# Kernel optimization log

Hardware: AMD Instinct MI355X
Metric: run time of the kernel (lower is better)

## Reference

```python
import jax, jax.numpy as jnp
import numpy as np

B, S, D, H = 2, 2048, 1024, 16
DK = D // H

def setup_inputs() -> dict:
    key = jax.random.key(0)
    ks = jax.random.split(key, 9)
    sc = 1.0 / np.sqrt(D)
    return {
        "query": jax.random.normal(ks[0], (B, S, D), jnp.float32),
        "key_": jax.random.normal(ks[1], (B, S, D), jnp.float32),
        "value": jax.random.normal(ks[2], (B, S, D), jnp.float32),
        "Wq": jax.random.normal(ks[3], (D, D), jnp.float32) * sc,
        "bq": jnp.zeros((D,), jnp.float32),
        "Wk": jax.random.normal(ks[4], (D, D), jnp.float32) * sc,
        "bk": jnp.zeros((D,), jnp.float32),
        "Wv": jax.random.normal(ks[5], (D, D), jnp.float32) * sc,
        "bv": jnp.zeros((D,), jnp.float32),
    }

def reference(query, key_, value, Wq, bq, Wk, bk, Wv, bv):
    # QKV projections -> [B, H, S, DK]
    def heads(x, W, b):
        return (x @ W + b).reshape(B, S, H, DK).transpose(0, 2, 1, 3)
    q = heads(query, Wq, bq)
    k = heads(key_, Wk, bk)
    v = heads(value, Wv, bv)
    scores = jnp.einsum('bhsd,bhtd->bhst', q, k) / jnp.sqrt(jnp.float32(DK))
    attn = jax.nn.softmax(scores, axis=-1)  # dropout = identity (eval)
    ctx = jnp.einsum('bhst,bhtd->bhsd', attn, v)
    return ctx.transpose(0, 2, 1, 3).reshape(B, S, D)
```

## Files before the change

### kernel.cpp

```cpp
#include <hip/hip_runtime.h>
#include <hip/hip_bf16.h>

typedef __bf16 bf16x4 __attribute__((ext_vector_type(4)));
typedef __bf16 bf16x8 __attribute__((ext_vector_type(8)));
typedef float  f32x4  __attribute__((ext_vector_type(4)));
typedef float  f32x16 __attribute__((ext_vector_type(16)));

constexpr int B = 2, S = 2048, D = 1024, H = 16, DK = 64;
constexpr int M = B * S;
constexpr int BH = B * H;

__device__ inline float fexp2(float x) {
#if __has_builtin(__builtin_amdgcn_exp2f)
  return __builtin_amdgcn_exp2f(x);
#else
  return exp2f(x);
#endif
}
__device__ inline float frcp(float x) {
#if __has_builtin(__builtin_amdgcn_rcpf)
  return __builtin_amdgcn_rcpf(x);
#else
  return 1.0f / x;
#endif
}
__device__ inline unsigned pk2(float lo, float hi) {
  union { __bf16 h[2]; unsigned u; } x;
  x.h[0] = (__bf16)lo; x.h[1] = (__bf16)hi;
  return x.u;
}

__global__ __launch_bounds__(256) void wtrans3(const float* __restrict__ w0,
                                               const float* __restrict__ w1,
                                               const float* __restrict__ w2,
                                               __bf16* __restrict__ t0,
                                               __bf16* __restrict__ t1,
                                               __bf16* __restrict__ t2) {
  int z = blockIdx.z;
  const float* W = z == 0 ? w0 : z == 1 ? w1 : w2;
  __bf16* WT = z == 0 ? t0 : z == 1 ? t1 : t2;
  __shared__ float t[32][33];
  int tx = threadIdx.x & 31, ty0 = threadIdx.x >> 5;
  int n0 = blockIdx.x * 32, k0 = blockIdx.y * 32;
#pragma unroll
  for (int i = 0; i < 4; ++i)
    t[ty0 + i * 8][tx] = W[(size_t)(k0 + ty0 + i * 8) * D + n0 + tx];
  __syncthreads();
#pragma unroll
  for (int i = 0; i < 4; ++i)
    WT[(size_t)(n0 + ty0 + i * 8) * D + k0 + tx] = (__bf16)t[tx][ty0 + i * 8];
}

constexpr int TM = 128, TN = 128, BK = 32;

__global__ __launch_bounds__(256, 3) void proj3(
    const float* __restrict__ X0, const float* __restrict__ X1,
    const float* __restrict__ X2, const __bf16* __restrict__ W0,
    const __bf16* __restrict__ W1, const __bf16* __restrict__ W2,
    const float* __restrict__ b0, const float* __restrict__ b1,
    const float* __restrict__ b2, __bf16* __restrict__ Qo,
    __bf16* __restrict__ Ko, __bf16* __restrict__ Vo) {
  __shared__ __align__(16) __bf16 As[TM * BK];
  __shared__ __align__(16) __bf16 Bs[TN * BK];
  int z = blockIdx.z;
  const float* A   = z == 0 ? X0 : z == 1 ? X1 : X2;
  const __bf16* BT = z == 0 ? W0 : z == 1 ? W1 : W2;
  const float* bias = z == 0 ? b0 : z == 1 ? b1 : b2;
  __bf16* out = z == 0 ? Qo : z == 1 ? Ko : Vo;
  int mode = (z == 2) ? 1 : 0;
  float osc = (z == 0) ? 0.18033688011112042f : 1.0f;

  int t = threadIdx.x;
  int fid = blockIdx.x;
  int xcd = fid & 7, slot = fid >> 3;
  int m0 = (xcd * 4 + (slot >> 3)) * TM;
  int n0 = (slot & 7) * TN;
  int w = t >> 6, lane = t & 63, c = lane & 15, g = lane >> 4;
  int wr = w >> 1, wc = w & 1;

  f32x4 acc[4][4];
#pragma unroll
  for (int i = 0; i < 4; ++i)
#pragma unroll
    for (int j = 0; j < 4; ++j) acc[i][j] = f32x4{0.f, 0.f, 0.f, 0.f};

  int srow = t >> 2;
  int scol = (t & 3) * 8;
  const float* ag = A + (size_t)(m0 + srow) * D + scol;
  const float* ag2 = ag + (size_t)64 * D;
  const __bf16* bg = BT + (size_t)(n0 + srow) * D + scol;

  float4 na0 = *(const float4*)(ag + 0);
  float4 na1 = *(const float4*)(ag + 4);
  float4 na2 = *(const float4*)(ag2 + 0);
  float4 na3 = *(const float4*)(ag2 + 4);

  for (int kk = 0; kk < D; kk += BK) {
    bf16x8 wa, wb;
    wa[0] = (__bf16)na0.x; wa[1] = (__bf16)na0.y; wa[2] = (__bf16)na0.z; wa[3] = (__bf16)na0.w;
    wa[4] = (__bf16)na1.x; wa[5] = (__bf16)na1.y; wa[6] = (__bf16)na1.z; wa[7] = (__bf16)na1.w;
    wb[0] = (__bf16)na2.x; wb[1] = (__bf16)na2.y; wb[2] = (__bf16)na2.z; wb[3] = (__bf16)na2.w;
    wb[4] = (__bf16)na3.x; wb[5] = (__bf16)na3.y; wb[6] = (__bf16)na3.z; wb[7] = (__bf16)na3.w;
    *(bf16x8*)(As + t * 8) = wa;
    *(bf16x8*)(As + 2048 + t * 8) = wb;
    __builtin_amdgcn_global_load_lds(
        (const __attribute__((address_space(1))) unsigned int*)(bg + kk),
        (__attribute__((address_space(3))) unsigned int*)(Bs + t * 8), 16, 0, 0);
    __builtin_amdgcn_global_load_lds(
        (const __attribute__((address_space(1))) unsigned int*)(bg + (size_t)64 * D + kk),
        (__attribute__((address_space(3))) unsigned int*)(Bs + 2048 + t * 8), 16, 0, 0);
    __syncthreads();

    if (kk + BK < D) {
      na0 = *(const float4*)(ag + kk + BK);
      na1 = *(const float4*)(ag + kk + BK + 4);
      na2 = *(const float4*)(ag2 + kk + BK);
      na3 = *(const float4*)(ag2 + kk + BK + 4);
    }

    bf16x8 af[4], bf[4];
#pragma unroll
    for (int i = 0; i < 4; ++i)
      af[i] = *(const bf16x8*)(As + (wr * 64 + i * 16 + c) * 32 + g * 8);
#pragma unroll
    for (int j = 0; j < 4; ++j)
      bf[j] = *(const bf16x8*)(Bs + (wc * 64 + j * 16 + c) * 32 + g * 8);
#pragma unroll
    for (int i = 0; i < 4; ++i)
#pragma unroll
      for (int j = 0; j < 4; ++j)
        acc[i][j] = __builtin_amdgcn_mfma_f32_16x16x32_bf16(af[i], bf[j], acc[i][j], 0, 0, 0);
    __syncthreads();
  }

#pragma unroll
  for (int i = 0; i < 4; ++i)
#pragma unroll
    for (int j = 0; j < 4; ++j) {
      int n = n0 + wc * 64 + j * 16 + c;
      float bv = bias[n];
      int h = n >> 6, dk = n & 63;
#pragma unroll
      for (int q = 0; q < 4; ++q) {
        int mrow = m0 + wr * 64 + i * 16 + g * 4 + q;
        int b = mrow >> 11, s = mrow & (S - 1);
        float val = (acc[i][j][q] + bv) * osc;
        size_t idx;
        if (mode == 0) idx = ((size_t)(b * H + h) * S + s) * DK + dk;
        else           idx = ((size_t)(b * H + h) * DK + dk) * S + s;
        out[idx] = (__bf16)val;
      }
    }
}

constexpr int NSTEP = S / 128;

__global__ __launch_bounds__(256) void attn(const __bf16* __restrict__ Q,
                                            const __bf16* __restrict__ K,
                                            const __bf16* __restrict__ VT,
                                            float* __restrict__ out) {
  __shared__ __align__(16) __bf16 Ks[2][8192];
  __shared__ __align__(16) __bf16 Vs[2][8192];

  int t = threadIdx.x, w = t >> 6, lane = t & 63;
  int l31 = lane & 31, hi = lane >> 5;

  int fid = blockIdx.x;
  int xcd = fid & 7, slot = fid >> 3;
  int bh = xcd * 4 + (slot >> 4);
  int q0 = (slot & 15) * 128 + w * 32;

  const __bf16* Qb = Q + (size_t)bh * S * DK;
  const char* Kg = (const char*)(K + (size_t)bh * S * DK);
  const char* Vg = (const char*)(VT + (size_t)bh * DK * S);

  bf16x8 qf[4];
  {
    const __bf16* qp = Qb + (size_t)(q0 + l31) * DK + hi * 8;
#pragma unroll
    for (int s2 = 0; s2 < 4; ++s2) qf[s2] = *(const bf16x8*)(qp + s2 * 16);
  }

  f32x16 acc0, acc1;
#pragma unroll
  for (int r = 0; r < 16; ++r) { acc0[r] = 0.f; acc1[r] = 0.f; }
  float lrun = 0.f;

  int krow = ((l31 >> 2) & 1) * 8 + ((l31 >> 3) & 1) * 16 + ((l31 >> 4) & 1) * 4 + (l31 & 3);
  int kswz = (((krow & 7) ^ ((krow >> 3) & 3)) << 4);
  int vswz = (((l31 & 7) ^ ((l31 >> 3) & 3)) << 4);

  auto stage = [&](int bufi, int kstep) {
#pragma unroll
    for (int i = 0; i < 4; ++i) {
      int L = i * 4096 + t * 16;
      {
        int row = L >> 7;
        int sz = (((row & 7) ^ ((row >> 3) & 3)) << 4);
        __builtin_amdgcn_global_load_lds(
            (const __attribute__((address_space(1))) unsigned int*)(Kg + (size_t)kstep * 16384 + (L ^ sz)),
            (__attribute__((address_space(3))) unsigned int*)((char*)&Ks[bufi][0] + L), 16, 0, 0);
      }
      {
        int row = L >> 8;
        int sz = (((row & 7) ^ ((row >> 3) & 3)) << 4);
        __builtin_amdgcn_global_load_lds(
            (const __attribute__((address_space(1))) unsigned int*)(Vg + (size_t)row * (S * 2) + kstep * 256 + ((L & 255) ^ sz)),
            (__attribute__((address_space(3))) unsigned int*)((char*)&Vs[bufi][0] + L), 16, 0, 0);
      }
    }
  };

  stage(0, 0);
  __syncthreads();

  for (int tt = 0; tt < NSTEP; ++tt) {
    int cur = tt & 1;
    if (tt + 1 < NSTEP) stage(cur ^ 1, tt + 1);
    const char* kb = (const char*)&Ks[cur][0];
    const char* vb = (const char*)&Vs[cur][0];

#pragma unroll
    for (int sub = 0; sub < 4; ++sub) {
      bf16x8 Kf[4], Vf[4];
      {
        const char* kr = kb + ((sub * 32 + krow) << 7);
#pragma unroll
        for (int s2 = 0; s2 < 4; ++s2)
          Kf[s2] = *(const bf16x8*)(kr + ((s2 * 32 + hi * 16) ^ kswz));
      }
#pragma unroll
      for (int ks = 0; ks < 2; ++ks)
#pragma unroll
        for (int db = 0; db < 2; ++db)
          Vf[ks * 2 + db] = *(const bf16x8*)(vb + ((db * 32 + l31) << 8) +
                                             ((sub * 64 + ks * 32 + hi * 16) ^ vswz));

      f32x16 st;
#pragma unroll
      for (int r = 0; r < 16; ++r) st[r] = 0.f;
#pragma unroll
      for (int s2 = 0; s2 < 4; ++s2)
        st = __builtin_amdgcn_mfma_f32_32x32x16_bf16(Kf[s2], qf[s2], st, 0, 0, 0);

      float p[16];
#pragma unroll
      for (int r = 0; r < 16; ++r) p[r] = fexp2(st[r]);
      {
        float t0 = (p[0] + p[1]) + (p[2] + p[3]);
        float t1 = (p[4] + p[5]) + (p[6] + p[7]);
        float t2 = (p[8] + p[9]) + (p[10] + p[11]);
        float t3 = (p[12] + p[13]) + (p[14] + p[15]);
        lrun += (t0 + t1) + (t2 + t3);
      }

      union Pk { unsigned u[4]; bf16x8 v; } P0, P1;
      P0.u[0] = pk2(p[0], p[1]);   P0.u[1] = pk2(p[2], p[3]);
      P0.u[2] = pk2(p[8], p[9]);   P0.u[3] = pk2(p[10], p[11]);
      P1.u[0] = pk2(p[4], p[5]);   P1.u[1] = pk2(p[6], p[7]);
      P1.u[2] = pk2(p[12], p[13]); P1.u[3] = pk2(p[14], p[15]);

      acc0 = __builtin_amdgcn_mfma_f32_32x32x16_bf16(P0.v, Vf[0], acc0, 0, 0, 0);
      acc1 = __builtin_amdgcn_mfma_f32_32x32x16_bf16(P0.v, Vf[1], acc1, 0, 0, 0);
      acc0 = __builtin_amdgcn_mfma_f32_32x32x16_bf16(P1.v, Vf[2], acc0, 0, 0, 0);
      acc1 = __builtin_amdgcn_mfma_f32_32x32x16_bf16(P1.v, Vf[3], acc1, 0, 0, 0);
    }
    __syncthreads();
  }

  lrun += __shfl_xor(lrun, 32);
  int b = bh >> 4, h = bh & 15;
#pragma unroll
  for (int r = 0; r < 16; ++r) {
    int rowq = (r & 3) + 8 * (r >> 2) + 4 * hi;
    float li = __shfl(lrun, rowq);
    float ri = frcp(li);
    size_t base = (size_t)(b * S + q0 + rowq) * D + h * 64 + l31;
    out[base] = acc0[r] * ri;
    out[base + 32] = acc1[r] * ri;
  }
}

extern "C" void kernel_launch(void* const* d_in, const int* in_sizes, int n_in,
                              void* d_out, int out_size, void* d_ws, size_t ws_size,
                              hipStream_t stream) {
  (void)in_sizes; (void)n_in; (void)out_size; (void)ws_size;
  const float* xq = (const float*)d_in[0];
  const float* xk = (const float*)d_in[1];
  const float* xv = (const float*)d_in[2];
  const float* Wq = (const float*)d_in[3];
  const float* bq = (const float*)d_in[4];
  const float* Wk = (const float*)d_in[5];
  const float* bk = (const float*)d_in[6];
  const float* Wv = (const float*)d_in[7];
  const float* bv = (const float*)d_in[8];

  char* ws = (char*)d_ws;
  const size_t MB = 1u << 20;
  __bf16* WT[3] = {(__bf16*)(ws + 24 * MB), (__bf16*)(ws + 26 * MB), (__bf16*)(ws + 28 * MB)};
  __bf16* Qb = (__bf16*)(ws + 30 * MB);
  __bf16* Kb = (__bf16*)(ws + 38 * MB);
  __bf16* Vt = (__bf16*)(ws + 46 * MB);

  wtrans3<<<dim3(D / 32, D / 32, 3), 256, 0, stream>>>(Wq, Wk, Wv, WT[0], WT[1], WT[2]);
  proj3<<<dim3(256, 1, 3), 256, 0, stream>>>(xq, xk, xv,
                                             WT[0], WT[1], WT[2],
                                             bq, bk, bv, Qb, Kb, Vt);
  attn<<<dim3(512), 256, 0, stream>>>(Qb, Kb, Vt, (float*)d_out);
}
```

Baseline: 105.6 us.

## Load K/V fragments directly from global into registers, dropping LDS staging

Replaces the double-buffered LDS staging of K and V tiles (global_load_lds plus barriers) with per-wave direct global-to-register loads of MFMA fragments, software-pipelined two tiles deep. This removes LDS traffic and block-level __syncthreads. In exchange, the four waves in a block now each fetch the same K/V data from global/L2, roughly quadrupling cache traffic, and the V loads are strided 16-byte accesses with less coalescing. It also raises register pressure.

```diff
diff --git a/kernel.cpp b/kernel.cpp
--- a/kernel.cpp
+++ b/kernel.cpp
@@ -153,15 +153,12 @@
     }
 }
 
-constexpr int NSTEP = S / 128;
+constexpr int NT = S / 32;
 
 __global__ __launch_bounds__(256) void attn(const __bf16* __restrict__ Q,
                                             const __bf16* __restrict__ K,
                                             const __bf16* __restrict__ VT,
                                             float* __restrict__ out) {
-  __shared__ __align__(16) __bf16 Ks[2][8192];
-  __shared__ __align__(16) __bf16 Vs[2][8192];
-
   int t = threadIdx.x, w = t >> 6, lane = t & 63;
   int l31 = lane & 31, hi = lane >> 5;
 
@@ -171,8 +168,8 @@
   int q0 = (slot & 15) * 128 + w * 32;
 
   const __bf16* Qb = Q + (size_t)bh * S * DK;
-  const char* Kg = (const char*)(K + (size_t)bh * S * DK);
-  const char* Vg = (const char*)(VT + (size_t)bh * DK * S);
+  const __bf16* Kb = K + (size_t)bh * S * DK;
+  const __bf16* Vb = VT + (size_t)bh * DK * S;
 
   bf16x8 qf[4];
   {
@@ -187,85 +184,60 @@
   float lrun = 0.f;
 
   int krow = ((l31 >> 2) & 1) * 8 + ((l31 >> 3) & 1) * 16 + ((l31 >> 4) & 1) * 4 + (l31 & 3);
-  int kswz = (((krow & 7) ^ ((krow >> 3) & 3)) << 4);
-  int vswz = (((l31 & 7) ^ ((l31 >> 3) & 3)) << 4);
-
-  auto stage = [&](int bufi, int kstep) {
-#pragma unroll
-    for (int i = 0; i < 4; ++i) {
-      int L = i * 4096 + t * 16;
-      {
-        int row = L >> 7;
-        int sz = (((row & 7) ^ ((row >> 3) & 3)) << 4);
-        __builtin_amdgcn_global_load_lds(
-            (const __attribute__((address_space(1))) unsigned int*)(Kg + (size_t)kstep * 16384 + (L ^ sz)),
-            (__attribute__((address_space(3))) unsigned int*)((char*)&Ks[bufi][0] + L), 16, 0, 0);
-      }
-      {
-        int row = L >> 8;
-        int sz = (((row & 7) ^ ((row >> 3) & 3)) << 4);
-        __builtin_amdgcn_global_load_lds(
-            (const __attribute__((address_space(1))) unsigned int*)(Vg + (size_t)row * (S * 2) + kstep * 256 + ((L & 255) ^ sz)),
-            (__attribute__((address_space(3))) unsigned int*)((char*)&Vs[bufi][0] + L), 16, 0, 0);
-      }
+
+  const __bf16* kp = Kb + (size_t)krow * DK + hi * 8;
+  const __bf16* vp0 = Vb + (size_t)l31 * S + hi * 8;
+  const __bf16* vp1 = Vb + (size_t)(32 + l31) * S + hi * 8;
+
+  auto loadKV = [&](int tt, bf16x8* Kf, bf16x8* Vf) {
+    const __bf16* kr = kp + (size_t)tt * 32 * DK;
+#pragma unroll
+    for (int s2 = 0; s2 < 4; ++s2) Kf[s2] = *(const bf16x8*)(kr + s2 * 16);
+    int c0 = tt * 32;
+    Vf[0] = *(const bf16x8*)(vp0 + c0);
+    Vf[1] = *(const bf16x8*)(vp1 + c0);
+    Vf[2] = *(const bf16x8*)(vp0 + c0 + 16);
+    Vf[3] = *(const bf16x8*)(vp1 + c0 + 16);
+  };
+
+  auto compute = [&](bf16x8* Kf, bf16x8* Vf) {
+    f32x16 st;
+#pragma unroll
+    for (int r = 0; r < 16; ++r) st[r] = 0.f;
+#pragma unroll
+    for (int s2 = 0; s2 < 4; ++s2)
+      st = __builtin_amdgcn_mfma_f32_32x32x16_bf16(Kf[s2], qf[s2], st, 0, 0, 0);
+
+    float p[16];
+#pragma unroll
+    for (int r = 0; r < 16; ++r) p[r] = fexp2(st[r]);
+    {
+      float t0 = (p[0] + p[1]) + (p[2] + p[3]);
+      float t1 = (p[4] + p[5]) + (p[6] + p[7]);
+      float t2 = (p[8] + p[9]) + (p[10] + p[11]);
+      float t3 = (p[12] + p[13]) + (p[14] + p[15]);
+      lrun += (t0 + t1) + (t2 + t3);
     }
+
+    union Pk { unsigned u[4]; bf16x8 v; } P0, P1;
+    P0.u[0] = pk2(p[0], p[1]);   P0.u[1] = pk2(p[2], p[3]);
+    P0.u[2] = pk2(p[8], p[9]);   P0.u[3] = pk2(p[10], p[11]);
+    P1.u[0] = pk2(p[4], p[5]);   P1.u[1] = pk2(p[6], p[7]);
+    P1.u[2] = pk2(p[12], p[13]); P1.u[3] = pk2(p[14], p[15]);
+
+    acc0 = __builtin_amdgcn_mfma_f32_32x32x16_bf16(P0.v, Vf[0], acc0, 0, 0, 0);
+    acc1 = __builtin_amdgcn_mfma_f32_32x32x16_bf16(P0.v, Vf[1], acc1, 0, 0, 0);
+    acc0 = __builtin_amdgcn_mfma_f32_32x32x16_bf16(P1.v, Vf[2], acc0, 0, 0, 0);
+    acc1 = __builtin_amdgcn_mfma_f32_32x32x16_bf16(P1.v, Vf[3], acc1, 0, 0, 0);
   };
 
-  stage(0, 0);
-  __syncthreads();
-
-  for (int tt = 0; tt < NSTEP; ++tt) {
-    int cur = tt & 1;
-    if (tt + 1 < NSTEP) stage(cur ^ 1, tt + 1);
-    const char* kb = (const char*)&Ks[cur][0];
-    const char* vb = (const char*)&Vs[cur][0];
-
-#pragma unroll
-    for (int sub = 0; sub < 4; ++sub) {
-      bf16x8 Kf[4], Vf[4];
-      {
-        const char* kr = kb + ((sub * 32 + krow) << 7);
-#pragma unroll
-        for (int s2 = 0; s2 < 4; ++s2)
-          Kf[s2] = *(const bf16x8*)(kr + ((s2 * 32 + hi * 16) ^ kswz));
-      }
-#pragma unroll
-      for (int ks = 0; ks < 2; ++ks)
-#pragma unroll
-        for (int db = 0; db < 2; ++db)
-          Vf[ks * 2 + db] = *(const bf16x8*)(vb + ((db * 32 + l31) << 8) +
-                                             ((sub * 64 + ks * 32 + hi * 16) ^ vswz));
-
-      f32x16 st;
-#pragma unroll
-      for (int r = 0; r < 16; ++r) st[r] = 0.f;
-#pragma unroll
-      for (int s2 = 0; s2 < 4; ++s2)
-        st = __builtin_amdgcn_mfma_f32_32x32x16_bf16(Kf[s2], qf[s2], st, 0, 0, 0);
-
-      float p[16];
-#pragma unroll
-      for (int r = 0; r < 16; ++r) p[r] = fexp2(st[r]);
-      {
-        float t0 = (p[0] + p[1]) + (p[2] + p[3]);
-        float t1 = (p[4] + p[5]) + (p[6] + p[7]);
-        float t2 = (p[8] + p[9]) + (p[10] + p[11]);
-        float t3 = (p[12] + p[13]) + (p[14] + p[15]);
-        lrun += (t0 + t1) + (t2 + t3);
-      }
-
-      union Pk { unsigned u[4]; bf16x8 v; } P0, P1;
-      P0.u[0] = pk2(p[0], p[1]);   P0.u[1] = pk2(p[2], p[3]);
-      P0.u[2] = pk2(p[8], p[9]);   P0.u[3] = pk2(p[10], p[11]);
-      P1.u[0] = pk2(p[4], p[5]);   P1.u[1] = pk2(p[6], p[7]);
-      P1.u[2] = pk2(p[12], p[13]); P1.u[3] = pk2(p[14], p[15]);
-
-      acc0 = __builtin_amdgcn_mfma_f32_32x32x16_bf16(P0.v, Vf[0], acc0, 0, 0, 0);
-      acc1 = __builtin_amdgcn_mfma_f32_32x32x16_bf16(P0.v, Vf[1], acc1, 0, 0, 0);
-      acc0 = __builtin_amdgcn_mfma_f32_32x32x16_bf16(P1.v, Vf[2], acc0, 0, 0, 0);
-      acc1 = __builtin_amdgcn_mfma_f32_32x32x16_bf16(P1.v, Vf[3], acc1, 0, 0, 0);
-    }
-    __syncthreads();
+  bf16x8 KA[4], VA[4], KB[4], VB[4];
+  loadKV(0, KA, VA);
+  for (int tt = 0; tt < NT; tt += 2) {
+    loadKV(tt + 1, KB, VB);
+    compute(KA, VA);
+    loadKV(tt + 2 < NT ? tt + 2 : NT - 1, KA, VA);
+    compute(KB, VB);
   }
 
   lrun += __shfl_xor(lrun, 32);
```

Measured after the change: 173.0 us. 1.64x slower.

## Double projection GEMM K-tile to 64 with XOR-swizzled LDS layout

Applied to the files above, without the earlier changes.

Raises the K step of the QKV projection GEMM from 32 to 64, so each barrier pair now covers twice as many MFMAs and the main loop runs half as many iterations. The LDS tiles are repacked as 128-byte rows, with an XOR swizzle on the 16-byte chunk index applied both when global data is staged and when fragments are read, to avoid bank conflicts. Each thread now holds 8 float4 prefetch registers instead of 4, and LDS use doubles to 32 KB per block. That adds register and occupancy pressure under the 3-blocks-per-SM launch bound.

```diff
diff --git a/kernel.cpp b/kernel.cpp
--- a/kernel.cpp
+++ b/kernel.cpp
@@ -51,7 +51,7 @@
     WT[(size_t)(n0 + ty0 + i * 8) * D + k0 + tx] = (__bf16)t[tx][ty0 + i * 8];
 }
 
-constexpr int TM = 128, TN = 128, BK = 32;
+constexpr int TM = 128, TN = 128, BK = 64;
 
 __global__ __launch_bounds__(256, 3) void proj3(
     const float* __restrict__ X0, const float* __restrict__ X1,
@@ -84,52 +84,66 @@
 #pragma unroll
     for (int j = 0; j < 4; ++j) acc[i][j] = f32x4{0.f, 0.f, 0.f, 0.f};
 
-  int srow = t >> 2;
-  int scol = (t & 3) * 8;
-  const float* ag = A + (size_t)(m0 + srow) * D + scol;
-  const float* ag2 = ag + (size_t)64 * D;
-  const __bf16* bg = BT + (size_t)(n0 + srow) * D + scol;
-
-  float4 na0 = *(const float4*)(ag + 0);
-  float4 na1 = *(const float4*)(ag + 4);
-  float4 na2 = *(const float4*)(ag2 + 0);
-  float4 na3 = *(const float4*)(ag2 + 4);
+  int srcoff = (((t & 7) ^ ((t >> 3) & 7)) << 4);
+  int srow = t >> 3;
+  const float* aptr[4];
+  const __bf16* bptr[4];
+#pragma unroll
+  for (int i = 0; i < 4; ++i) {
+    aptr[i] = A + (size_t)(m0 + i * 32 + srow) * D + (srcoff >> 1);
+    bptr[i] = BT + (size_t)(n0 + i * 32 + srow) * D + (srcoff >> 1);
+  }
+
+  float4 pa[4][2];
+#pragma unroll
+  for (int i = 0; i < 4; ++i) {
+    pa[i][0] = *(const float4*)(aptr[i]);
+    pa[i][1] = *(const float4*)(aptr[i] + 4);
+  }
+
+  int rswz = ((c & 7) << 4);
 
   for (int kk = 0; kk < D; kk += BK) {
-    bf16x8 wa, wb;
-    wa[0] = (__bf16)na0.x; wa[1] = (__bf16)na0.y; wa[2] = (__bf16)na0.z; wa[3] = (__bf16)na0.w;
-    wa[4] = (__bf16)na1.x; wa[5] = (__bf16)na1.y; wa[6] = (__bf16)na1.z; wa[7] = (__bf16)na1.w;
-    wb[0] = (__bf16)na2.x; wb[1] = (__bf16)na2.y; wb[2] = (__bf16)na2.z; wb[3] = (__bf16)na2.w;
-    wb[4] = (__bf16)na3.x; wb[5] = (__bf16)na3.y; wb[6] = (__bf16)na3.z; wb[7] = (__bf16)na3.w;
-    *(bf16x8*)(As + t * 8) = wa;
-    *(bf16x8*)(As + 2048 + t * 8) = wb;
-    __builtin_amdgcn_global_load_lds(
-        (const __attribute__((address_space(1))) unsigned int*)(bg + kk),
-        (__attribute__((address_space(3))) unsigned int*)(Bs + t * 8), 16, 0, 0);
-    __builtin_amdgcn_global_load_lds(
-        (const __attribute__((address_space(1))) unsigned int*)(bg + (size_t)64 * D + kk),
-        (__attribute__((address_space(3))) unsigned int*)(Bs + 2048 + t * 8), 16, 0, 0);
+#pragma unroll
+    for (int i = 0; i < 4; ++i) {
+      bf16x8 v;
+      v[0] = (__bf16)pa[i][0].x; v[1] = (__bf16)pa[i][0].y;
+      v[2] = (__bf16)pa[i][0].z; v[3] = (__bf16)pa[i][0].w;
+      v[4] = (__bf16)pa[i][1].x; v[5] = (__bf16)pa[i][1].y;
+      v[6] = (__bf16)pa[i][1].z; v[7] = (__bf16)pa[i][1].w;
+      *(bf16x8*)((char*)As + i * 4096 + t * 16) = v;
+    }
+#pragma unroll
+    for (int i = 0; i < 4; ++i)
+      __builtin_amdgcn_global_load_lds(
+          (const __attribute__((address_space(1))) unsigned int*)(bptr[i] + kk),
+          (__attribute__((address_space(3))) unsigned int*)((char*)Bs + i * 4096 + t * 16), 16, 0, 0);
     __syncthreads();
 
     if (kk + BK < D) {
-      na0 = *(const float4*)(ag + kk + BK);
-      na1 = *(const float4*)(ag + kk + BK + 4);
-      na2 = *(const float4*)(ag2 + kk + BK);
-      na3 = *(const float4*)(ag2 + kk + BK + 4);
-    }
-
-    bf16x8 af[4], bf[4];
-#pragma unroll
-    for (int i = 0; i < 4; ++i)
-      af[i] = *(const bf16x8*)(As + (wr * 64 + i * 16 + c) * 32 + g * 8);
-#pragma unroll
-    for (int j = 0; j < 4; ++j)
-      bf[j] = *(const bf16x8*)(Bs + (wc * 64 + j * 16 + c) * 32 + g * 8);
-#pragma unroll
-    for (int i = 0; i < 4; ++i)
+#pragma unroll
+      for (int i = 0; i < 4; ++i) {
+        pa[i][0] = *(const float4*)(aptr[i] + kk + BK);
+        pa[i][1] = *(const float4*)(aptr[i] + kk + BK + 4);
+      }
+    }
+
+#pragma unroll
+    for (int ks = 0; ks < 2; ++ks) {
+      int cb = (ks * 64 + g * 16) ^ rswz;
+      bf16x8 af[4], bf[4];
+#pragma unroll
+      for (int i = 0; i < 4; ++i)
+        af[i] = *(const bf16x8*)((char*)As + (wr * 64 + i * 16 + c) * 128 + cb);
 #pragma unroll
       for (int j = 0; j < 4; ++j)
-        acc[i][j] = __builtin_amdgcn_mfma_f32_16x16x32_bf16(af[i], bf[j], acc[i][j], 0, 0, 0);
+        bf[j] = *(const bf16x8*)((char*)Bs + (wc * 64 + j * 16 + c) * 128 + cb);
+#pragma unroll
+      for (int i = 0; i < 4; ++i)
+#pragma unroll
+        for (int j = 0; j < 4; ++j)
+          acc[i][j] = __builtin_amdgcn_mfma_f32_16x16x32_bf16(af[i], bf[j], acc[i][j], 0, 0, 0);
+    }
     __syncthreads();
   }
 
```

Result: faster. 100.6 us (-4.7%).
